# Performance work log

Measured on AMD Instinct MI355X. Metric: run time of the kernel, lower is better.

Reference implementation:

```python
import jax, jax.numpy as jnp
import numpy as np

N_NODES = 100000
N_EDGES = 1600000
D_IN = 128
D_HID = 128
D_OUT = 64


def setup_inputs() -> dict:
    key = jax.random.key(0)
    ks = jax.random.split(key, 8)
    x = jax.random.normal(ks[0], (N_NODES, D_IN), dtype=jnp.float32)
    edge_index = jax.random.randint(ks[1], (2, N_EDGES), 0, N_NODES, dtype=jnp.int64)
    s1 = 1.0 / np.sqrt(D_IN)
    s2 = 1.0 / np.sqrt(D_HID)
    W1 = jax.random.uniform(ks[2], (D_IN, D_HID), jnp.float32, -s1, s1)
    b1 = jnp.zeros((D_HID,), jnp.float32)
    W2 = jax.random.uniform(ks[3], (D_HID, D_HID), jnp.float32, -s2, s2)
    b2 = jnp.zeros((D_HID,), jnp.float32)
    fc_W = jax.random.uniform(ks[4], (D_HID, D_OUT), jnp.float32, -s2, s2)
    fc_b = jax.random.uniform(ks[5], (D_OUT,), jnp.float32, -s2, s2)
    return {"x": x, "edge_index": edge_index, "W1": W1, "b1": b1,
            "W2": W2, "b2": b2, "fc_W": fc_W, "fc_b": fc_b}


def _gcn_norm(edge_index, n_nodes):
    # add self-loops, compute symmetric normalization D^{-1/2} A D^{-1/2}
    loops = jnp.arange(n_nodes, dtype=edge_index.dtype)
    src = jnp.concatenate([edge_index[0], loops])  # [E+N]
    dst = jnp.concatenate([edge_index[1], loops])
    ones = jnp.ones(src.shape[0], jnp.float32)
    deg = jax.ops.segment_sum(ones, dst, num_segments=n_nodes)  # [N]
    dinv = 1.0 / jnp.sqrt(deg)  # deg >= 1 thanks to self-loops
    norm = dinv[src] * dinv[dst]  # [E+N]
    return src, dst, norm


def _gcn_conv(x, W, b, src, dst, norm, n_nodes):
    h = x @ W                                  # [N, d]
    msg = h[src] * norm[:, None]               # gather + scale, [E+N, d]
    out = jax.ops.segment_sum(msg, dst, num_segments=n_nodes)  # scatter-add
    return out + b


def reference(x, edge_index, W1, b1, W2, b2, fc_W, fc_b):
    n = x.shape[0]
    src, dst, norm = _gcn_norm(edge_index, n)
    h = jax.nn.relu(_gcn_conv(x, W1, b1, src, dst, norm, n))
    # dropout is identity in inference mode
    h = jax.nn.relu(_gcn_conv(h, W2, b2, src, dst, norm, n))
    return h @ fc_W + fc_b
```

## Files before the change

### kernel.cpp

```cpp
#include <hip/hip_runtime.h>

typedef __attribute__((ext_vector_type(8))) short bf16x8;
typedef __attribute__((ext_vector_type(4))) float f32x4;

__device__ __forceinline__ unsigned short f2bf(float x) {
  union { float f; unsigned u; } v; v.f = x;
  return (unsigned short)((v.u + 0x7fffu + ((v.u >> 16) & 1u)) >> 16);
}
__device__ __forceinline__ float bf2f(unsigned short h) {
  union { unsigned u; float f; } v; v.u = ((unsigned)h) << 16; return v.f;
}


__global__ __launch_bounds__(256) void bhist_k(const int* __restrict__ dst,
                                               int* __restrict__ bcnt, int E, int B) {
  __shared__ int h[512];
  for (int i = threadIdx.x; i < B; i += 256) h[i] = 0;
  __syncthreads();
  for (int e = blockIdx.x * 256 + threadIdx.x; e < E; e += gridDim.x * 256)
    atomicAdd(&h[dst[e] >> 8], 1);
  __syncthreads();
  for (int i = threadIdx.x; i < B; i += 256)
    if (h[i]) atomicAdd(&bcnt[i * 16], h[i]);
}

__global__ __launch_bounds__(512) void bscan_k(const int* __restrict__ bcnt,
                                               int* __restrict__ bstart,
                                               int* __restrict__ bfill,
                                               int* __restrict__ row_start,
                                               int B, int N, int E) {
  __shared__ int sd[512];
  int t = threadIdx.x;
  int v = (t < B) ? bcnt[t * 16] : 0;
  sd[t] = v; __syncthreads();
  for (int off = 1; off < 512; off <<= 1) {
    int x = (t >= off) ? sd[t - off] : 0;
    __syncthreads();
    sd[t] += x;
    __syncthreads();
  }
  if (t < B) {
    int excl = sd[t] - v;
    bstart[t] = excl;
    bfill[t * 16] = excl;
  }
  if (t == 0) { bstart[B] = E; row_start[N] = E; }
}

__global__ __launch_bounds__(256) void bin_k(const int* __restrict__ src,
                                             const int* __restrict__ dst,
                                             int* __restrict__ bfill,
                                             unsigned* __restrict__ ebuf, int E, int B) {
  __shared__ int hist[512];
  __shared__ int base[512];
  int t = threadIdx.x;
  int chunk = (E + gridDim.x - 1) / gridDim.x;
  int e0 = blockIdx.x * chunk;
  int e1 = e0 + chunk; if (e1 > E) e1 = E;
  for (int i = t; i < B; i += 256) hist[i] = 0;
  __syncthreads();
  for (int e = e0 + t; e < e1; e += 256) atomicAdd(&hist[dst[e] >> 8], 1);
  __syncthreads();
  for (int i = t; i < B; i += 256) {
    int c = hist[i];
    base[i] = c ? atomicAdd(&bfill[i * 16], c) : 0;
  }
  __syncthreads();
  for (int e = e0 + t; e < e1; e += 256) {
    int d = dst[e];
    int b = d >> 8;
    int pos = atomicAdd(&base[b], 1);
    ebuf[pos] = ((unsigned)(d & 255) << 17) | (unsigned)src[e];
  }
}

__global__ __launch_bounds__(256) void bsort_k(const unsigned* __restrict__ ebuf,
                                               const int* __restrict__ bstart,
                                               int* __restrict__ csr,
                                               int* __restrict__ row_start,
                                               float* __restrict__ dinv, int N) {
  __shared__ int cnt[256];
  __shared__ int sd[256];
  __shared__ int ofs[256];
  __shared__ int sorted[8192];
  int b = blockIdx.x, t = threadIdx.x;
  int bs = bstart[b], be = bstart[b + 1];
  int m = be - bs;
  if (m > 8192) m = 8192;
  cnt[t] = 0;
  __syncthreads();
  for (int i = t; i < m; i += 256) atomicAdd(&cnt[ebuf[bs + i] >> 17], 1);
  __syncthreads();
  int deg = cnt[t];
  sd[t] = deg; __syncthreads();
  for (int off = 1; off < 256; off <<= 1) {
    int x = (t >= off) ? sd[t - off] : 0;
    __syncthreads();
    sd[t] += x;
    __syncthreads();
  }
  int excl = sd[t] - deg;
  ofs[t] = excl;
  int node = (b << 8) + t;
  if (node < N) {
    row_start[node] = bs + excl;
    dinv[node] = rsqrtf((float)(deg + 1));
  }
  __syncthreads();
  for (int i = t; i < m; i += 256) {
    unsigned r = ebuf[bs + i];
    int d = r >> 17;
    int p = atomicAdd(&ofs[d], 1);
    if (p < 8192) sorted[p] = (int)(r & 0x1FFFFu);
  }
  __syncthreads();
  for (int i = t; i < m; i += 256) csr[bs + i] = sorted[i];
}

__global__ __launch_bounds__(256) void wfill_k(const int* __restrict__ csr,
                                               const float* __restrict__ dinv,
                                               int2* __restrict__ csrw, int E) {
  int e = blockIdx.x * 256 + threadIdx.x;
  if (e < E) {
    int s = csr[e];
    csrw[e] = make_int2(s, __float_as_int(dinv[s]));
  }
}

template <int NCOL, bool INF32, bool OUTF32>
__global__ __launch_bounds__(256) void gemm_k(const void* __restrict__ Ap,
                                              const float* __restrict__ W,
                                              const float* __restrict__ bias,
                                              void* __restrict__ Cp, int M) {
  __shared__ __align__(16) unsigned short Ws[NCOL * 136];
  int tid = threadIdx.x;
  for (int e = tid; e < 128 * NCOL; e += 256) {
    int k = e / NCOL, n = e % NCOL;
    Ws[n * 136 + k] = f2bf(W[e]);
  }
  __syncthreads();

  int wave = tid >> 6, lane = tid & 63;
  int q = lane >> 4, r = lane & 15;
  const int NT = NCOL / 16;
  int ntile = M >> 4;
  for (int tile = blockIdx.x * 4 + wave; tile < ntile; tile += gridDim.x * 4) {
    int row = tile * 16 + r;
    bf16x8 a[4];
    if (INF32) {
      const float* A = (const float*)Ap + (size_t)row * 128 + q * 8;
#pragma unroll
      for (int kk = 0; kk < 4; kk++) {
        const float4* p = (const float4*)(A + kk * 32);
        float4 f0 = p[0], f1 = p[1];
        bf16x8 tt;
        tt[0] = (short)f2bf(f0.x); tt[1] = (short)f2bf(f0.y);
        tt[2] = (short)f2bf(f0.z); tt[3] = (short)f2bf(f0.w);
        tt[4] = (short)f2bf(f1.x); tt[5] = (short)f2bf(f1.y);
        tt[6] = (short)f2bf(f1.z); tt[7] = (short)f2bf(f1.w);
        a[kk] = tt;
      }
    } else {
      const unsigned short* A = (const unsigned short*)Ap + (size_t)row * 128 + q * 8;
#pragma unroll
      for (int kk = 0; kk < 4; kk++) a[kk] = *(const bf16x8*)(A + kk * 32);
    }
    f32x4 acc[NT];
#pragma unroll
    for (int nt = 0; nt < NT; nt++) { acc[nt][0] = 0.f; acc[nt][1] = 0.f; acc[nt][2] = 0.f; acc[nt][3] = 0.f; }
#pragma unroll
    for (int kk = 0; kk < 4; kk++) {
#pragma unroll
      for (int nt = 0; nt < NT; nt++) {
        bf16x8 bfr = *(const bf16x8*)&Ws[(nt * 16 + r) * 136 + kk * 32 + q * 8];
        acc[nt] = __builtin_amdgcn_mfma_f32_16x16x32_bf16(a[kk], bfr, acc[nt], 0, 0, 0);
      }
    }
#pragma unroll
    for (int nt = 0; nt < NT; nt++) {
#pragma unroll
      for (int rr = 0; rr < 4; rr++) {
        int orow = tile * 16 + q * 4 + rr;
        int ocol = nt * 16 + r;
        if (OUTF32)
          ((float*)Cp)[(size_t)orow * NCOL + ocol] = acc[nt][rr] + bias[ocol];
        else
          ((unsigned short*)Cp)[(size_t)orow * NCOL + ocol] = f2bf(acc[nt][rr]);
      }
    }
  }
}

__global__ __launch_bounds__(256) void agg_k(const unsigned short* __restrict__ h,
                                             const float* __restrict__ dinv,
                                             const int* __restrict__ row_start,
                                             const int2* __restrict__ csrw,
                                             const float* __restrict__ bias,
                                             unsigned short* __restrict__ out, int N) {
  int lane = threadIdx.x & 63;
  int node = (blockIdx.x * 256 + threadIdx.x) >> 6;
  if (node >= N) return;
  int g = lane >> 4, r = lane & 15;
  float di = dinv[node];
  int beg = row_start[node];
  int deg = row_start[node + 1] - beg;

  float acc[8];
#pragma unroll
  for (int i = 0; i < 8; i++) acc[i] = 0.f;

  for (int base = -1; base < deg; base += 64) {
    int idx = base + lane;
    int s = node; float wv = 0.f;
    if (idx < 0) { wv = di; }
    else if (idx < deg) {
      int2 rec = csrw[beg + idx];
      s = rec.x; wv = __int_as_float(rec.y);
    }
    int cntv = deg - base; if (cntv > 64) cntv = 64;
    int j = 0;
    for (; j + 8 <= cntv; j += 8) {
      int sj0 = __shfl(s, j + g);
      float wj0 = __shfl(wv, j + g);
      int sj1 = __shfl(s, j + 4 + g);
      float wj1 = __shfl(wv, j + 4 + g);
      bf16x8 h0 = *(const bf16x8*)(h + (size_t)sj0 * 128 + r * 8);
      bf16x8 h1 = *(const bf16x8*)(h + (size_t)sj1 * 128 + r * 8);
#pragma unroll
      for (int i = 0; i < 8; i++) acc[i] += bf2f((unsigned short)h0[i]) * wj0;
#pragma unroll
      for (int i = 0; i < 8; i++) acc[i] += bf2f((unsigned short)h1[i]) * wj1;
    }
    for (; j < cntv; j += 4) {
      int sj = __shfl(s, j + g);
      float wj = __shfl(wv, j + g);
      bf16x8 hv = *(const bf16x8*)(h + (size_t)sj * 128 + r * 8);
#pragma unroll
      for (int i = 0; i < 8; i++) acc[i] += bf2f((unsigned short)hv[i]) * wj;
    }
  }

#pragma unroll
  for (int i = 0; i < 8; i++) {
    acc[i] += __shfl_xor(acc[i], 16);
    acc[i] += __shfl_xor(acc[i], 32);
  }

  if (g == 0) {
    bf16x8 t;
#pragma unroll
    for (int i = 0; i < 8; i++) {
      float v = acc[i] * di + bias[r * 8 + i];
      if (v < 0.f) v = 0.f;
      t[i] = (short)f2bf(v);
    }
    *(bf16x8*)(out + (size_t)node * 128 + r * 8) = t;
  }
}

extern "C" void kernel_launch(void* const* d_in, const int* in_sizes, int n_in,
                              void* d_out, int out_size, void* d_ws, size_t ws_size,
                              hipStream_t stream) {
  const float* x  = (const float*)d_in[0];
  const int* ei   = (const int*)d_in[1];
  const float* W1 = (const float*)d_in[2];
  const float* b1 = (const float*)d_in[3];
  const float* W2 = (const float*)d_in[4];
  const float* b2 = (const float*)d_in[5];
  const float* fcW = (const float*)d_in[6];
  const float* fcb = (const float*)d_in[7];
  float* out = (float*)d_out;

  int N = in_sizes[0] / 128;
  int E = in_sizes[1] / 2;
  int B = (N + 255) >> 8;
  const int* src = ei;
  const int* dst = ei + E;

  char* w = (char*)d_ws;
  auto alloc = [&](size_t b) { char* p = w; w += (b + 255) & ~(size_t)255; return p; };
  float* dinv      = (float*)alloc((size_t)N * 4);
  int*   row_start = (int*)alloc((size_t)(N + 1) * 4);
  int*   bcnt      = (int*)alloc((size_t)(B + 1) * 64);
  int*   bstart    = (int*)alloc((size_t)(B + 1) * 4);
  int*   bfill     = (int*)alloc((size_t)(B + 1) * 64);
  unsigned* ebuf   = (unsigned*)alloc((size_t)E * 4);
  int*   csr       = (int*)alloc((size_t)E * 4);
  int2*  csrw      = (int2*)alloc((size_t)E * 8);
  unsigned short* bufA = (unsigned short*)alloc((size_t)N * 128 * 2);
  unsigned short* bufB = (unsigned short*)alloc((size_t)N * 128 * 2);

  hipMemsetAsync(bcnt, 0, (size_t)(B + 1) * 64, stream);

  bhist_k<<<256, 256, 0, stream>>>(dst, bcnt, E, B);
  bscan_k<<<1, 512, 0, stream>>>(bcnt, bstart, bfill, row_start, B, N, E);
  bin_k<<<256, 256, 0, stream>>>(src, dst, bfill, ebuf, E, B);
  bsort_k<<<B, 256, 0, stream>>>(ebuf, bstart, csr, row_start, dinv, N);
  wfill_k<<<(E + 255) / 256, 256, 0, stream>>>(csr, dinv, csrw, E);

  gemm_k<128, true, false><<<512, 256, 0, stream>>>((const void*)x, W1, nullptr, (void*)bufA, N);
  agg_k<<<(N + 3) / 4, 256, 0, stream>>>(bufA, dinv, row_start, csrw, b1, bufB, N);
  gemm_k<128, false, false><<<512, 256, 0, stream>>>((const void*)bufB, W2, nullptr, (void*)bufA, N);
  agg_k<<<(N + 3) / 4, 256, 0, stream>>>(bufA, dinv, row_start, csrw, b2, bufB, N);
  gemm_k<64, false, true><<<512, 256, 0, stream>>>((const void*)bufB, fcW, fcb, (void*)out, N);
}
```

Baseline: 337.7 us.

## Fuse bucket scan into bin and sort kernels; vectorize bf16 aggregation

Removes the single-block bscan_k launch by having bin_k and bsort_k each recompute the bucket-count prefix scan redundantly in shared memory, and merges the counter buffers into one memset. The aggregation kernel now unpacks bf16 with bit ops into float2 vectors for packed FMA and unrolls the neighbor loop to four outstanding gathers per lane group. This trades one kernel launch and serialization point for redundant scans in every block, and raises memory-level parallelism in the gather loop at some register cost.

```diff
diff --git a/kernel.cpp b/kernel.cpp
--- a/kernel.cpp
+++ b/kernel.cpp
@@ -2,6 +2,7 @@
 
 typedef __attribute__((ext_vector_type(8))) short bf16x8;
 typedef __attribute__((ext_vector_type(4))) float f32x4;
+typedef __attribute__((ext_vector_type(2))) float f32x2;
 
 __device__ __forceinline__ unsigned short f2bf(float x) {
   union { float f; unsigned u; } v; v.f = x;
@@ -24,36 +25,31 @@
     if (h[i]) atomicAdd(&bcnt[i * 16], h[i]);
 }
 
-__global__ __launch_bounds__(512) void bscan_k(const int* __restrict__ bcnt,
-                                               int* __restrict__ bstart,
-                                               int* __restrict__ bfill,
-                                               int* __restrict__ row_start,
-                                               int B, int N, int E) {
-  __shared__ int sd[512];
-  int t = threadIdx.x;
-  int v = (t < B) ? bcnt[t * 16] : 0;
-  sd[t] = v; __syncthreads();
-  for (int off = 1; off < 512; off <<= 1) {
-    int x = (t >= off) ? sd[t - off] : 0;
-    __syncthreads();
-    sd[t] += x;
-    __syncthreads();
-  }
-  if (t < B) {
-    int excl = sd[t] - v;
-    bstart[t] = excl;
-    bfill[t * 16] = excl;
-  }
-  if (t == 0) { bstart[B] = E; row_start[N] = E; }
-}
-
 __global__ __launch_bounds__(256) void bin_k(const int* __restrict__ src,
                                              const int* __restrict__ dst,
+                                             const int* __restrict__ bcnt,
                                              int* __restrict__ bfill,
                                              unsigned* __restrict__ ebuf, int E, int B) {
   __shared__ int hist[512];
   __shared__ int base[512];
+  __shared__ int sd[256];
   int t = threadIdx.x;
+  int i0 = 2 * t, i1 = 2 * t + 1;
+  int v0 = (i0 < B) ? bcnt[i0 * 16] : 0;
+  int v1 = (i1 < B) ? bcnt[i1 * 16] : 0;
+  int ts = v0 + v1;
+  sd[t] = ts; __syncthreads();
+  for (int off = 1; off < 256; off <<= 1) {
+    int x = (t >= off) ? sd[t - off] : 0;
+    __syncthreads();
+    sd[t] += x;
+    __syncthreads();
+  }
+  int excl = sd[t] - ts;
+  base[i0] = excl;
+  base[i1] = excl + v0;
+  __syncthreads();
+
   int chunk = (E + gridDim.x - 1) / gridDim.x;
   int e0 = blockIdx.x * chunk;
   int e1 = e0 + chunk; if (e1 > E) e1 = E;
@@ -63,30 +59,47 @@
   __syncthreads();
   for (int i = t; i < B; i += 256) {
     int c = hist[i];
-    base[i] = c ? atomicAdd(&bfill[i * 16], c) : 0;
+    hist[i] = base[i] + (c ? atomicAdd(&bfill[i * 16], c) : 0);
   }
   __syncthreads();
   for (int e = e0 + t; e < e1; e += 256) {
     int d = dst[e];
     int b = d >> 8;
-    int pos = atomicAdd(&base[b], 1);
+    int pos = atomicAdd(&hist[b], 1);
     ebuf[pos] = ((unsigned)(d & 255) << 17) | (unsigned)src[e];
   }
 }
 
 __global__ __launch_bounds__(256) void bsort_k(const unsigned* __restrict__ ebuf,
-                                               const int* __restrict__ bstart,
+                                               const int* __restrict__ bcnt,
                                                int* __restrict__ csr,
                                                int* __restrict__ row_start,
-                                               float* __restrict__ dinv, int N) {
+                                               float* __restrict__ dinv, int N, int B, int E) {
   __shared__ int cnt[256];
   __shared__ int sd[256];
   __shared__ int ofs[256];
   __shared__ int sorted[8192];
+  __shared__ int s_bs, s_m;
   int b = blockIdx.x, t = threadIdx.x;
-  int bs = bstart[b], be = bstart[b + 1];
-  int m = be - bs;
+  int i0 = 2 * t, i1 = 2 * t + 1;
+  int v0 = (i0 < B) ? bcnt[i0 * 16] : 0;
+  int v1 = (i1 < B) ? bcnt[i1 * 16] : 0;
+  int ts = v0 + v1;
+  sd[t] = ts; __syncthreads();
+  for (int off = 1; off < 256; off <<= 1) {
+    int x = (t >= off) ? sd[t - off] : 0;
+    __syncthreads();
+    sd[t] += x;
+    __syncthreads();
+  }
+  int excl = sd[t] - ts;
+  if (i0 == b) { s_bs = excl; s_m = v0; }
+  if (i1 == b) { s_bs = excl + v0; s_m = v1; }
+  if (b == 0 && t == 0) row_start[N] = E;
+  __syncthreads();
+  int bs = s_bs, m = s_m;
   if (m > 8192) m = 8192;
+
   cnt[t] = 0;
   __syncthreads();
   for (int i = t; i < m; i += 256) atomicAdd(&cnt[ebuf[bs + i] >> 17], 1);
@@ -99,11 +112,11 @@
     sd[t] += x;
     __syncthreads();
   }
-  int excl = sd[t] - deg;
-  ofs[t] = excl;
+  int nexcl = sd[t] - deg;
+  ofs[t] = nexcl;
   int node = (b << 8) + t;
   if (node < N) {
-    row_start[node] = bs + excl;
+    row_start[node] = bs + nexcl;
     dinv[node] = rsqrtf((float)(deg + 1));
   }
   __syncthreads();
@@ -205,9 +218,25 @@
   int beg = row_start[node];
   int deg = row_start[node + 1] - beg;
 
-  float acc[8];
-#pragma unroll
-  for (int i = 0; i < 8; i++) acc[i] = 0.f;
+  f32x2 acc2[4];
+#pragma unroll
+  for (int i = 0; i < 4; i++) { acc2[i][0] = 0.f; acc2[i][1] = 0.f; }
+
+#define ACC8(U, WV)                                                            \
+  {                                                                            \
+    f32x2 w2; w2[0] = (WV); w2[1] = (WV);                                      \
+    f32x2 p0, p1, p2, p3;                                                      \
+    p0[0] = __uint_as_float((U).x << 16);                                      \
+    p0[1] = __uint_as_float((U).x & 0xffff0000u);                              \
+    p1[0] = __uint_as_float((U).y << 16);                                      \
+    p1[1] = __uint_as_float((U).y & 0xffff0000u);                              \
+    p2[0] = __uint_as_float((U).z << 16);                                      \
+    p2[1] = __uint_as_float((U).z & 0xffff0000u);                              \
+    p3[0] = __uint_as_float((U).w << 16);                                      \
+    p3[1] = __uint_as_float((U).w & 0xffff0000u);                              \
+    acc2[0] += p0 * w2; acc2[1] += p1 * w2;                                    \
+    acc2[2] += p2 * w2; acc2[3] += p3 * w2;                                    \
+  }
 
   for (int base = -1; base < deg; base += 64) {
     int idx = base + lane;
@@ -219,38 +248,40 @@
     }
     int cntv = deg - base; if (cntv > 64) cntv = 64;
     int j = 0;
-    for (; j + 8 <= cntv; j += 8) {
-      int sj0 = __shfl(s, j + g);
-      float wj0 = __shfl(wv, j + g);
-      int sj1 = __shfl(s, j + 4 + g);
-      float wj1 = __shfl(wv, j + 4 + g);
-      bf16x8 h0 = *(const bf16x8*)(h + (size_t)sj0 * 128 + r * 8);
-      bf16x8 h1 = *(const bf16x8*)(h + (size_t)sj1 * 128 + r * 8);
-#pragma unroll
-      for (int i = 0; i < 8; i++) acc[i] += bf2f((unsigned short)h0[i]) * wj0;
-#pragma unroll
-      for (int i = 0; i < 8; i++) acc[i] += bf2f((unsigned short)h1[i]) * wj1;
+    for (; j + 16 <= cntv; j += 16) {
+      int s0 = __shfl(s, j + g);       float w0 = __shfl(wv, j + g);
+      int s1 = __shfl(s, j + 4 + g);   float w1 = __shfl(wv, j + 4 + g);
+      int s2 = __shfl(s, j + 8 + g);   float w2_ = __shfl(wv, j + 8 + g);
+      int s3 = __shfl(s, j + 12 + g);  float w3 = __shfl(wv, j + 12 + g);
+      uint4 u0 = *(const uint4*)(h + (size_t)s0 * 128 + r * 8);
+      uint4 u1 = *(const uint4*)(h + (size_t)s1 * 128 + r * 8);
+      uint4 u2 = *(const uint4*)(h + (size_t)s2 * 128 + r * 8);
+      uint4 u3 = *(const uint4*)(h + (size_t)s3 * 128 + r * 8);
+      ACC8(u0, w0); ACC8(u1, w1); ACC8(u2, w2_); ACC8(u3, w3);
     }
     for (; j < cntv; j += 4) {
       int sj = __shfl(s, j + g);
       float wj = __shfl(wv, j + g);
-      bf16x8 hv = *(const bf16x8*)(h + (size_t)sj * 128 + r * 8);
-#pragma unroll
-      for (int i = 0; i < 8; i++) acc[i] += bf2f((unsigned short)hv[i]) * wj;
-    }
-  }
-
+      uint4 u = *(const uint4*)(h + (size_t)sj * 128 + r * 8);
+      ACC8(u, wj);
+    }
+  }
+#undef ACC8
+
+  float a[8];
+#pragma unroll
+  for (int d = 0; d < 4; d++) { a[2 * d] = acc2[d][0]; a[2 * d + 1] = acc2[d][1]; }
 #pragma unroll
   for (int i = 0; i < 8; i++) {
-    acc[i] += __shfl_xor(acc[i], 16);
-    acc[i] += __shfl_xor(acc[i], 32);
+    a[i] += __shfl_xor(a[i], 16);
+    a[i] += __shfl_xor(a[i], 32);
   }
 
   if (g == 0) {
     bf16x8 t;
 #pragma unroll
     for (int i = 0; i < 8; i++) {
-      float v = acc[i] * di + bias[r * 8 + i];
+      float v = a[i] * di + bias[r * 8 + i];
       if (v < 0.f) v = 0.f;
       t[i] = (short)f2bf(v);
     }
@@ -281,21 +312,20 @@
   auto alloc = [&](size_t b) { char* p = w; w += (b + 255) & ~(size_t)255; return p; };
   float* dinv      = (float*)alloc((size_t)N * 4);
   int*   row_start = (int*)alloc((size_t)(N + 1) * 4);
-  int*   bcnt      = (int*)alloc((size_t)(B + 1) * 64);
-  int*   bstart    = (int*)alloc((size_t)(B + 1) * 4);
-  int*   bfill     = (int*)alloc((size_t)(B + 1) * 64);
+  int*   batom     = (int*)alloc((size_t)(B + 1) * 128);
+  int*   bcnt      = batom;
+  int*   bfill     = batom + (size_t)(B + 1) * 16;
   unsigned* ebuf   = (unsigned*)alloc((size_t)E * 4);
   int*   csr       = (int*)alloc((size_t)E * 4);
   int2*  csrw      = (int2*)alloc((size_t)E * 8);
   unsigned short* bufA = (unsigned short*)alloc((size_t)N * 128 * 2);
   unsigned short* bufB = (unsigned short*)alloc((size_t)N * 128 * 2);
 
-  hipMemsetAsync(bcnt, 0, (size_t)(B + 1) * 64, stream);
+  hipMemsetAsync(batom, 0, (size_t)(B + 1) * 128, stream);
 
   bhist_k<<<256, 256, 0, stream>>>(dst, bcnt, E, B);
-  bscan_k<<<1, 512, 0, stream>>>(bcnt, bstart, bfill, row_start, B, N, E);
-  bin_k<<<256, 256, 0, stream>>>(src, dst, bfill, ebuf, E, B);
-  bsort_k<<<B, 256, 0, stream>>>(ebuf, bstart, csr, row_start, dinv, N);
+  bin_k<<<256, 256, 0, stream>>>(src, dst, bcnt, bfill, ebuf, E, B);
+  bsort_k<<<B, 256, 0, stream>>>(ebuf, bcnt, csr, row_start, dinv, N, B, E);
   wfill_k<<<(E + 255) / 256, 256, 0, stream>>>(csr, dinv, csrw, E);
 
   gemm_k<128, true, false><<<512, 256, 0, stream>>>((const void*)x, W1, nullptr, (void*)bufA, N);
```

Result: slower. 347.0 us (+2.7%).
